# Kernel tuning notes

Hardware: AMD Instinct MI355X
Metric: run time of the kernel (lower is better)

The kernel has to match this reference:

```python
import jax, jax.numpy as jnp
import numpy as np

LN_EPS = 1e-5
NUM_EXPERTS = 8

def setup_inputs() -> dict:
    key = jax.random.key(0)
    ks = jax.random.split(key, 8)
    B, S, D = 8, 2048, 2048
    R = D // 4  # reduced_dim = 512
    E = NUM_EXPERTS
    scale1 = 1.0 / np.sqrt(D)
    scale2 = 1.0 / np.sqrt(R)
    return {
        "hidden_states": jax.random.normal(ks[0], (B, S, D), dtype=jnp.float32),
        "ln_gamma": jnp.ones((D,), dtype=jnp.float32),
        "ln_beta": jnp.zeros((D,), dtype=jnp.float32),
        "w1": jax.random.uniform(ks[1], (D, R), minval=-scale1, maxval=scale1, dtype=jnp.float32),
        "b1": jax.random.uniform(ks[2], (R,), minval=-scale1, maxval=scale1, dtype=jnp.float32),
        "w2": jax.random.uniform(ks[3], (R, R), minval=-scale2, maxval=scale2, dtype=jnp.float32),
        "b2": jax.random.uniform(ks[4], (R,), minval=-scale2, maxval=scale2, dtype=jnp.float32),
        "wr": jax.random.uniform(ks[5], (R, E), minval=-scale2, maxval=scale2, dtype=jnp.float32),
        "br": jax.random.uniform(ks[6], (E,), minval=-scale2, maxval=scale2, dtype=jnp.float32),
    }

def reference(hidden_states, ln_gamma, ln_beta, w1, b1, w2, b2, wr, br):
    # LayerNorm over last dim (eps matches torch default 1e-5)
    mu = jnp.mean(hidden_states, axis=-1, keepdims=True)
    var = jnp.mean(jnp.square(hidden_states - mu), axis=-1, keepdims=True)
    x = (hidden_states - mu) * jax.lax.rsqrt(var + LN_EPS) * ln_gamma + ln_beta
    # Linear -> GELU (exact, torch default) -> Linear
    h = jax.nn.gelu(jnp.einsum('bsd,dr->bsr', x, w1) + b1, approximate=False)
    t = jnp.einsum('bsr,rq->bsq', h, w2) + b2  # [B,S,R]
    batch_reduced = jnp.sum(t, axis=1)          # [B,R]
    router_logits = batch_reduced @ wr + br     # [B,E]
    # top-1 expert per batch element; one-hot targets via scatter
    expert_indices = jnp.argmax(router_logits, axis=-1)                 # [B]
    targets = jax.nn.one_hot(expert_indices, router_logits.shape[-1],
                             dtype=router_logits.dtype)                 # [B,E]
    # BCE-with-logits, mean over all elements: log(1+e^x) - x*t
    aux_loss = jnp.mean(jnp.logaddexp(0.0, router_logits) - router_logits * targets)
    # mode over batch of top-1 indices (torch .mode returns smallest on ties;
    # argmax of bincount picks the first/smallest max index -> matches)
    counts = jnp.sum(targets, axis=0)
    next_idx = jnp.argmax(counts)
    return aux_loss, next_idx
```

## Files before the change

kernel.cpp:

```cpp
#include <hip/hip_runtime.h>
#include <math.h>

#define D_DIM 2048
#define R_DIM 512
#define E_NUM 8
#define B_NUM 8
#define S_NUM 2048
#define M_DIM 16384
#define LN_EPS 1e-5f

typedef __attribute__((ext_vector_type(8))) short bf16x8;
typedef __attribute__((ext_vector_type(4))) float f32x4;

__device__ __forceinline__ unsigned short f2bf(float f) {
    unsigned u = __float_as_uint(f);
    return (unsigned short)((u + 0x7FFFu + ((u >> 16) & 1u)) >> 16);
}
__device__ __forceinline__ float bf2f(unsigned short h) {
    return __uint_as_float(((unsigned)h) << 16);
}

__device__ __forceinline__ void gload_lds16(const void* g, void* l) {
    __builtin_amdgcn_global_load_lds(
        (const __attribute__((address_space(1))) void*)g,
        (__attribute__((address_space(3))) void*)l, 16, 0, 0);
}

__global__ __launch_bounds__(256) void ln_split_kernel(float* __restrict__ x,
                                                       const float* __restrict__ gamma,
                                                       const float* __restrict__ beta) {
    __shared__ float sred[8];
    const int t = threadIdx.x;
    float* row = x + (size_t)blockIdx.x * D_DIM;
    const float4 v0  = ((const float4*)row)[t];
    const float4 v1  = ((const float4*)row)[t + 256];
    const float4 g0  = ((const float4*)gamma)[t];
    const float4 g1  = ((const float4*)gamma)[t + 256];
    const float4 be0 = ((const float4*)beta)[t];
    const float4 be1 = ((const float4*)beta)[t + 256];

    float s  = v0.x + v0.y + v0.z + v0.w + v1.x + v1.y + v1.z + v1.w;
    float sq = v0.x*v0.x + v0.y*v0.y + v0.z*v0.z + v0.w*v0.w
             + v1.x*v1.x + v1.y*v1.y + v1.z*v1.z + v1.w*v1.w;
#pragma unroll
    for (int off = 32; off > 0; off >>= 1) {
        s  += __shfl_down(s, off);
        sq += __shfl_down(sq, off);
    }
    if ((t & 63) == 0) { sred[(t >> 6) * 2] = s; sred[(t >> 6) * 2 + 1] = sq; }
    __syncthreads();
    s  = sred[0] + sred[2] + sred[4] + sred[6];
    sq = sred[1] + sred[3] + sred[5] + sred[7];
    const float mu  = s * (1.f / D_DIM);
    const float var = sq * (1.f / D_DIM) - mu * mu;
    const float rs  = rsqrtf(var + LN_EPS);

    ushort4 h0, h1;
    h0.x = f2bf(fmaf((v0.x - mu) * rs, g0.x, be0.x));
    h0.y = f2bf(fmaf((v0.y - mu) * rs, g0.y, be0.y));
    h0.z = f2bf(fmaf((v0.z - mu) * rs, g0.z, be0.z));
    h0.w = f2bf(fmaf((v0.w - mu) * rs, g0.w, be0.w));
    h1.x = f2bf(fmaf((v1.x - mu) * rs, g1.x, be1.x));
    h1.y = f2bf(fmaf((v1.y - mu) * rs, g1.y, be1.y));
    h1.z = f2bf(fmaf((v1.z - mu) * rs, g1.z, be1.z));
    h1.w = f2bf(fmaf((v1.w - mu) * rs, g1.w, be1.w));

    ushort4* rowu = (ushort4*)row;
    rowu[t]       = h0;
    rowu[t + 256] = h1;
}

__global__ __launch_bounds__(256) void wsplit_kernel(const float* __restrict__ w1,
                                                     unsigned short* __restrict__ wt_hi,
                                                     unsigned short* __restrict__ wt_lo) {
    const int tid = blockIdx.x * 256 + threadIdx.x;
    const int n  = tid >> 9;
    const int k4 = tid & 511;
    ushort4 h, l;
    unsigned short hh;
    float f;
    f = w1[(size_t)(k4 * 4 + 0) * R_DIM + n]; hh = f2bf(f); h.x = hh; l.x = f2bf(f - bf2f(hh));
    f = w1[(size_t)(k4 * 4 + 1) * R_DIM + n]; hh = f2bf(f); h.y = hh; l.y = f2bf(f - bf2f(hh));
    f = w1[(size_t)(k4 * 4 + 2) * R_DIM + n]; hh = f2bf(f); h.z = hh; l.z = f2bf(f - bf2f(hh));
    f = w1[(size_t)(k4 * 4 + 3) * R_DIM + n]; hh = f2bf(f); h.w = hh; l.w = f2bf(f - bf2f(hh));
    ((ushort4*)wt_hi)[(size_t)n * 512 + k4] = h;
    ((ushort4*)wt_lo)[(size_t)n * 512 + k4] = l;
}

#define BM 128
#define BN 128
#define BK 64

__global__ __launch_bounds__(256, 2) void gemm_kernel(
    const unsigned short* __restrict__ xs,
    const unsigned short* __restrict__ wt_hi,
    const unsigned short* __restrict__ wt_lo,
    const float* __restrict__ b1,
    float* __restrict__ hsum) {
    __shared__ __align__(16) unsigned short lds[3 * 8192];

    const int t = threadIdx.x, lane = t & 63, wid = t >> 6;
    const int xcd = blockIdx.x & 7, i0 = blockIdx.x >> 3;
    const int n0 = (xcd >> 1) * BN;
    const int m0 = ((xcd & 1) * 64 + i0) * BM;
    const int mw = wid >> 1, nw = wid & 1;
    const int fr = lane & 15, kg = lane >> 4, fr7 = lane & 7;

    f32x4 acc[4][4];
#pragma unroll
    for (int i = 0; i < 4; ++i)
#pragma unroll
        for (int j = 0; j < 4; ++j) acc[i][j] = (f32x4){0.f, 0.f, 0.f, 0.f};

    int srow[4], sgo[4], ldso[4];
#pragma unroll
    for (int ii = 0; ii < 4; ++ii) {
        const int idx = wid * 4 + ii;
        const int o = (idx << 10) + (lane << 4);
        const int r = o >> 7, sl = (o >> 4) & 7;
        srow[ii] = r;
        sgo[ii]  = ((sl ^ (r & 7)) << 4);
        ldso[ii] = (idx << 10);
    }

    int aoff[4], boff[4];
#pragma unroll
    for (int f = 0; f < 4; ++f) {
        aoff[f] = (mw * 64 + f * 16 + fr) * 128;
        boff[f] = (nw * 64 + f * 16 + fr) * 128;
    }
    const char* ldsb = (const char*)lds;

    for (int k0b = 0; k0b < D_DIM * 2; k0b += BK * 2) {
        __syncthreads();
#pragma unroll
        for (int ii = 0; ii < 4; ++ii) {
            const char* a  = (const char*)xs    + (size_t)(m0 + srow[ii]) * 8192 + k0b + sgo[ii];
            const char* bh = (const char*)wt_hi + (size_t)(n0 + srow[ii]) * 4096 + k0b + sgo[ii];
            const char* bl = (const char*)wt_lo + (size_t)(n0 + srow[ii]) * 4096 + k0b + sgo[ii];
            gload_lds16(a,  (char*)lds +     0 + ldso[ii]);
            gload_lds16(bh, (char*)lds + 16384 + ldso[ii]);
            gload_lds16(bl, (char*)lds + 32768 + ldso[ii]);
        }
        __syncthreads();
#pragma unroll
        for (int kk = 0; kk < 2; ++kk) {
            const int sw = ((kk * 4 + kg) ^ fr7) << 4;
            bf16x8 ah[4], bh[4], bl[4];
#pragma unroll
            for (int f = 0; f < 4; ++f) {
                ah[f] = *(const bf16x8*)(ldsb +     0 + aoff[f] + sw);
                bh[f] = *(const bf16x8*)(ldsb + 16384 + boff[f] + sw);
                bl[f] = *(const bf16x8*)(ldsb + 32768 + boff[f] + sw);
            }
#pragma unroll
            for (int i = 0; i < 4; ++i)
#pragma unroll
                for (int j = 0; j < 4; ++j) {
                    acc[i][j] = __builtin_amdgcn_mfma_f32_16x16x32_bf16(ah[i], bh[j], acc[i][j], 0, 0, 0);
                    acc[i][j] = __builtin_amdgcn_mfma_f32_16x16x32_bf16(ah[i], bl[j], acc[i][j], 0, 0, 0);
                }
        }
    }

    __syncthreads();
    float* red = (float*)lds;
    float pn[4];
#pragma unroll
    for (int j = 0; j < 4; ++j) pn[j] = 0.f;
#pragma unroll
    for (int j = 0; j < 4; ++j) {
        const float bb = b1[n0 + nw * 64 + j * 16 + fr];
#pragma unroll
        for (int i = 0; i < 4; ++i)
#pragma unroll
            for (int r = 0; r < 4; ++r) {
                const float y = acc[i][j][r] + bb;
                pn[j] += 0.5f * y * (1.f + erff(y * 0.70710678118654752f));
            }
    }
#pragma unroll
    for (int j = 0; j < 4; ++j)
        red[(wid * 4 + kg) * 64 + j * 16 + fr] = pn[j];
    __syncthreads();
    if (t < 128) {
        const int nw2 = t >> 6, cl = t & 63;
        float s2 = 0.f;
#pragma unroll
        for (int mw2 = 0; mw2 < 2; ++mw2)
#pragma unroll
            for (int g = 0; g < 4; ++g)
                s2 += red[((mw2 * 2 + nw2) * 4 + g) * 64 + cl];
        atomicAdd(&hsum[(m0 >> 11) * R_DIM + n0 + t], s2);
    }
}

__global__ void router1_kernel(const float* __restrict__ hsum,
                               const float* __restrict__ w2,
                               float* __restrict__ brd) {
    const int q  = blockIdx.x * 64 + threadIdx.x;
    const int r0 = blockIdx.y * 64;
    float acc[8] = {0, 0, 0, 0, 0, 0, 0, 0};
    for (int r = r0 + threadIdx.y; r < r0 + 64; r += 4) {
        const float w = w2[(size_t)r * R_DIM + q];
#pragma unroll
        for (int b = 0; b < 8; ++b) acc[b] = fmaf(hsum[b * R_DIM + r], w, acc[b]);
    }
    __shared__ float sred[4][8][64];
#pragma unroll
    for (int b = 0; b < 8; ++b) sred[threadIdx.y][b][threadIdx.x] = acc[b];
    __syncthreads();
    if (threadIdx.y == 0) {
#pragma unroll
        for (int b = 0; b < 8; ++b) {
            float s = sred[0][b][threadIdx.x] + sred[1][b][threadIdx.x]
                    + sred[2][b][threadIdx.x] + sred[3][b][threadIdx.x];
            atomicAdd(&brd[b * R_DIM + q], s);
        }
    }
}

__global__ void router2_kernel(const float* __restrict__ brd,
                               const float* __restrict__ b2,
                               const float* __restrict__ wr,
                               const float* __restrict__ br,
                               float* __restrict__ out) {
    __shared__ float lg[64];
    const int t = threadIdx.x;
    const int b = t >> 3, e = t & 7;
    float s = br[e];
    for (int q = 0; q < R_DIM; ++q) {
        const float v = fmaf((float)S_NUM, b2[q], brd[b * R_DIM + q]);
        s = fmaf(v, wr[q * E_NUM + e], s);
    }
    lg[t] = s;
    __syncthreads();
    if (t == 0) {
        int cnt[8] = {0, 0, 0, 0, 0, 0, 0, 0};
        float loss = 0.f;
        for (int bb = 0; bb < 8; ++bb) {
            int best = 0;
            float bv = lg[bb * 8];
            for (int ee = 1; ee < 8; ++ee)
                if (lg[bb * 8 + ee] > bv) { bv = lg[bb * 8 + ee]; best = ee; }
            cnt[best]++;
            for (int ee = 0; ee < 8; ++ee) {
                const float xv = lg[bb * 8 + ee];
                loss += fmaxf(xv, 0.f) + log1pf(expf(-fabsf(xv))) - (ee == best ? xv : 0.f);
            }
        }
        out[0] = loss * (1.f / 64.f);
        int ni = 0;
        for (int ee = 1; ee < 8; ++ee)
            if (cnt[ee] > cnt[ni]) ni = ee;
        out[1] = (float)ni;
    }
}

extern "C" void kernel_launch(void* const* d_in, const int* in_sizes, int n_in,
                              void* d_out, int out_size, void* d_ws, size_t ws_size,
                              hipStream_t stream) {
    float* x           = (float*)d_in[0];
    const float* gamma = (const float*)d_in[1];
    const float* beta  = (const float*)d_in[2];
    const float* w1    = (const float*)d_in[3];
    const float* b1    = (const float*)d_in[4];
    const float* w2    = (const float*)d_in[5];
    const float* b2    = (const float*)d_in[6];
    const float* wr    = (const float*)d_in[7];
    const float* br    = (const float*)d_in[8];
    float* out = (float*)d_out;
    float* ws  = (float*)d_ws;

    float* hsum = ws;
    float* brd  = ws + 4096;
    unsigned short* wt_hi = (unsigned short*)(ws + 8192);
    unsigned short* wt_lo = wt_hi + (size_t)R_DIM * D_DIM;

    hipMemsetAsync(ws, 0, 8192 * sizeof(float), stream);
    ln_split_kernel<<<dim3(M_DIM), dim3(256), 0, stream>>>(x, gamma, beta);
    wsplit_kernel<<<dim3(1024), dim3(256), 0, stream>>>(w1, wt_hi, wt_lo);
    gemm_kernel<<<dim3(512), dim3(256), 0, stream>>>(
        (const unsigned short*)x, wt_hi, wt_lo, b1, hsum);
    router1_kernel<<<dim3(8, 8), dim3(64, 4), 0, stream>>>(hsum, w2, brd);
    router2_kernel<<<dim3(1), dim3(64), 0, stream>>>(brd, b2, wr, br, out);
}
```

Baseline: 334.5 us.

## Drop bf16 hi/lo weight split, fuse prep kernels, parallelize router reduction

The weight matrix is now rounded to a single bf16 copy instead of a hi/lo pair, which halves the MFMA count, the B-tile loads and the LDS footprint in the GEMM. LayerNorm, the weight conversion and workspace zeroing are merged into one prep kernel, replacing a memset and two launches. The b2 bias is folded into router1, and router2 splits its dot products across 8 thread groups. The cost is lower weight precision, which could flip an argmax in routing when logits are close.

```diff
diff --git a/kernel.cpp b/kernel.cpp
--- a/kernel.cpp
+++ b/kernel.cpp
@@ -16,9 +16,6 @@
     unsigned u = __float_as_uint(f);
     return (unsigned short)((u + 0x7FFFu + ((u >> 16) & 1u)) >> 16);
 }
-__device__ __forceinline__ float bf2f(unsigned short h) {
-    return __uint_as_float(((unsigned)h) << 16);
-}
 
 __device__ __forceinline__ void gload_lds16(const void* g, void* l) {
     __builtin_amdgcn_global_load_lds(
@@ -26,65 +23,65 @@
         (__attribute__((address_space(3))) void*)l, 16, 0, 0);
 }
 
-__global__ __launch_bounds__(256) void ln_split_kernel(float* __restrict__ x,
-                                                       const float* __restrict__ gamma,
-                                                       const float* __restrict__ beta) {
-    __shared__ float sred[8];
+__global__ __launch_bounds__(256) void prep_kernel(float* __restrict__ x,
+                                                   const float* __restrict__ gamma,
+                                                   const float* __restrict__ beta,
+                                                   const float* __restrict__ w1,
+                                                   unsigned short* __restrict__ wt,
+                                                   float* __restrict__ zbuf) {
     const int t = threadIdx.x;
-    float* row = x + (size_t)blockIdx.x * D_DIM;
-    const float4 v0  = ((const float4*)row)[t];
-    const float4 v1  = ((const float4*)row)[t + 256];
-    const float4 g0  = ((const float4*)gamma)[t];
-    const float4 g1  = ((const float4*)gamma)[t + 256];
-    const float4 be0 = ((const float4*)beta)[t];
-    const float4 be1 = ((const float4*)beta)[t + 256];
-
-    float s  = v0.x + v0.y + v0.z + v0.w + v1.x + v1.y + v1.z + v1.w;
-    float sq = v0.x*v0.x + v0.y*v0.y + v0.z*v0.z + v0.w*v0.w
-             + v1.x*v1.x + v1.y*v1.y + v1.z*v1.z + v1.w*v1.w;
-#pragma unroll
-    for (int off = 32; off > 0; off >>= 1) {
-        s  += __shfl_down(s, off);
-        sq += __shfl_down(sq, off);
-    }
-    if ((t & 63) == 0) { sred[(t >> 6) * 2] = s; sred[(t >> 6) * 2 + 1] = sq; }
-    __syncthreads();
-    s  = sred[0] + sred[2] + sred[4] + sred[6];
-    sq = sred[1] + sred[3] + sred[5] + sred[7];
-    const float mu  = s * (1.f / D_DIM);
-    const float var = sq * (1.f / D_DIM) - mu * mu;
-    const float rs  = rsqrtf(var + LN_EPS);
-
-    ushort4 h0, h1;
-    h0.x = f2bf(fmaf((v0.x - mu) * rs, g0.x, be0.x));
-    h0.y = f2bf(fmaf((v0.y - mu) * rs, g0.y, be0.y));
-    h0.z = f2bf(fmaf((v0.z - mu) * rs, g0.z, be0.z));
-    h0.w = f2bf(fmaf((v0.w - mu) * rs, g0.w, be0.w));
-    h1.x = f2bf(fmaf((v1.x - mu) * rs, g1.x, be1.x));
-    h1.y = f2bf(fmaf((v1.y - mu) * rs, g1.y, be1.y));
-    h1.z = f2bf(fmaf((v1.z - mu) * rs, g1.z, be1.z));
-    h1.w = f2bf(fmaf((v1.w - mu) * rs, g1.w, be1.w));
-
-    ushort4* rowu = (ushort4*)row;
-    rowu[t]       = h0;
-    rowu[t + 256] = h1;
-}
-
-__global__ __launch_bounds__(256) void wsplit_kernel(const float* __restrict__ w1,
-                                                     unsigned short* __restrict__ wt_hi,
-                                                     unsigned short* __restrict__ wt_lo) {
-    const int tid = blockIdx.x * 256 + threadIdx.x;
-    const int n  = tid >> 9;
-    const int k4 = tid & 511;
-    ushort4 h, l;
-    unsigned short hh;
-    float f;
-    f = w1[(size_t)(k4 * 4 + 0) * R_DIM + n]; hh = f2bf(f); h.x = hh; l.x = f2bf(f - bf2f(hh));
-    f = w1[(size_t)(k4 * 4 + 1) * R_DIM + n]; hh = f2bf(f); h.y = hh; l.y = f2bf(f - bf2f(hh));
-    f = w1[(size_t)(k4 * 4 + 2) * R_DIM + n]; hh = f2bf(f); h.z = hh; l.z = f2bf(f - bf2f(hh));
-    f = w1[(size_t)(k4 * 4 + 3) * R_DIM + n]; hh = f2bf(f); h.w = hh; l.w = f2bf(f - bf2f(hh));
-    ((ushort4*)wt_hi)[(size_t)n * 512 + k4] = h;
-    ((ushort4*)wt_lo)[(size_t)n * 512 + k4] = l;
+    if (blockIdx.x < M_DIM) {
+        __shared__ float sred[8];
+        float* row = x + (size_t)blockIdx.x * D_DIM;
+        const float4 v0  = ((const float4*)row)[t];
+        const float4 v1  = ((const float4*)row)[t + 256];
+        const float4 g0  = ((const float4*)gamma)[t];
+        const float4 g1  = ((const float4*)gamma)[t + 256];
+        const float4 be0 = ((const float4*)beta)[t];
+        const float4 be1 = ((const float4*)beta)[t + 256];
+
+        float s  = v0.x + v0.y + v0.z + v0.w + v1.x + v1.y + v1.z + v1.w;
+        float sq = v0.x*v0.x + v0.y*v0.y + v0.z*v0.z + v0.w*v0.w
+                 + v1.x*v1.x + v1.y*v1.y + v1.z*v1.z + v1.w*v1.w;
+#pragma unroll
+        for (int off = 32; off > 0; off >>= 1) {
+            s  += __shfl_down(s, off);
+            sq += __shfl_down(sq, off);
+        }
+        if ((t & 63) == 0) { sred[(t >> 6) * 2] = s; sred[(t >> 6) * 2 + 1] = sq; }
+        __syncthreads();
+        s  = sred[0] + sred[2] + sred[4] + sred[6];
+        sq = sred[1] + sred[3] + sred[5] + sred[7];
+        const float mu  = s * (1.f / D_DIM);
+        const float var = sq * (1.f / D_DIM) - mu * mu;
+        const float rs  = rsqrtf(var + LN_EPS);
+
+        ushort4 h0, h1;
+        h0.x = f2bf(fmaf((v0.x - mu) * rs, g0.x, be0.x));
+        h0.y = f2bf(fmaf((v0.y - mu) * rs, g0.y, be0.y));
+        h0.z = f2bf(fmaf((v0.z - mu) * rs, g0.z, be0.z));
+        h0.w = f2bf(fmaf((v0.w - mu) * rs, g0.w, be0.w));
+        h1.x = f2bf(fmaf((v1.x - mu) * rs, g1.x, be1.x));
+        h1.y = f2bf(fmaf((v1.y - mu) * rs, g1.y, be1.y));
+        h1.z = f2bf(fmaf((v1.z - mu) * rs, g1.z, be1.z));
+        h1.w = f2bf(fmaf((v1.w - mu) * rs, g1.w, be1.w));
+
+        ushort4* rowu = (ushort4*)row;
+        rowu[t]       = h0;
+        rowu[t + 256] = h1;
+    } else if (blockIdx.x < M_DIM + 1024) {
+        const int tid = (blockIdx.x - M_DIM) * 256 + t;
+        const int n  = tid >> 9;
+        const int k4 = tid & 511;
+        ushort4 h;
+        h.x = f2bf(w1[(size_t)(k4 * 4 + 0) * R_DIM + n]);
+        h.y = f2bf(w1[(size_t)(k4 * 4 + 1) * R_DIM + n]);
+        h.z = f2bf(w1[(size_t)(k4 * 4 + 2) * R_DIM + n]);
+        h.w = f2bf(w1[(size_t)(k4 * 4 + 3) * R_DIM + n]);
+        ((ushort4*)wt)[(size_t)n * 512 + k4] = h;
+    } else {
+        zbuf[(blockIdx.x - M_DIM - 1024) * 256 + t] = 0.f;
+    }
 }
 
 #define BM 128
@@ -93,11 +90,10 @@
 
 __global__ __launch_bounds__(256, 2) void gemm_kernel(
     const unsigned short* __restrict__ xs,
-    const unsigned short* __restrict__ wt_hi,
-    const unsigned short* __restrict__ wt_lo,
+    const unsigned short* __restrict__ wt,
     const float* __restrict__ b1,
     float* __restrict__ hsum) {
-    __shared__ __align__(16) unsigned short lds[3 * 8192];
+    __shared__ __align__(16) unsigned short lds[2 * 8192];
 
     const int t = threadIdx.x, lane = t & 63, wid = t >> 6;
     const int xcd = blockIdx.x & 7, i0 = blockIdx.x >> 3;
@@ -135,31 +131,26 @@
         __syncthreads();
 #pragma unroll
         for (int ii = 0; ii < 4; ++ii) {
-            const char* a  = (const char*)xs    + (size_t)(m0 + srow[ii]) * 8192 + k0b + sgo[ii];
-            const char* bh = (const char*)wt_hi + (size_t)(n0 + srow[ii]) * 4096 + k0b + sgo[ii];
-            const char* bl = (const char*)wt_lo + (size_t)(n0 + srow[ii]) * 4096 + k0b + sgo[ii];
-            gload_lds16(a,  (char*)lds +     0 + ldso[ii]);
-            gload_lds16(bh, (char*)lds + 16384 + ldso[ii]);
-            gload_lds16(bl, (char*)lds + 32768 + ldso[ii]);
+            const char* a = (const char*)xs + (size_t)(m0 + srow[ii]) * 8192 + k0b + sgo[ii];
+            const char* b = (const char*)wt + (size_t)(n0 + srow[ii]) * 4096 + k0b + sgo[ii];
+            gload_lds16(a, (char*)lds +     0 + ldso[ii]);
+            gload_lds16(b, (char*)lds + 16384 + ldso[ii]);
         }
         __syncthreads();
 #pragma unroll
         for (int kk = 0; kk < 2; ++kk) {
             const int sw = ((kk * 4 + kg) ^ fr7) << 4;
-            bf16x8 ah[4], bh[4], bl[4];
+            bf16x8 ah[4], bh[4];
 #pragma unroll
             for (int f = 0; f < 4; ++f) {
                 ah[f] = *(const bf16x8*)(ldsb +     0 + aoff[f] + sw);
                 bh[f] = *(const bf16x8*)(ldsb + 16384 + boff[f] + sw);
-                bl[f] = *(const bf16x8*)(ldsb + 32768 + boff[f] + sw);
             }
 #pragma unroll
             for (int i = 0; i < 4; ++i)
 #pragma unroll
-                for (int j = 0; j < 4; ++j) {
+                for (int j = 0; j < 4; ++j)
                     acc[i][j] = __builtin_amdgcn_mfma_f32_16x16x32_bf16(ah[i], bh[j], acc[i][j], 0, 0, 0);
-                    acc[i][j] = __builtin_amdgcn_mfma_f32_16x16x32_bf16(ah[i], bl[j], acc[i][j], 0, 0, 0);
-                }
         }
     }
 
@@ -197,6 +188,7 @@
 
 __global__ void router1_kernel(const float* __restrict__ hsum,
                                const float* __restrict__ w2,
+                               const float* __restrict__ b2,
                                float* __restrict__ brd) {
     const int q  = blockIdx.x * 64 + threadIdx.x;
     const int r0 = blockIdx.y * 64;
@@ -211,31 +203,38 @@
     for (int b = 0; b < 8; ++b) sred[threadIdx.y][b][threadIdx.x] = acc[b];
     __syncthreads();
     if (threadIdx.y == 0) {
+        const float bias2 = (blockIdx.y == 0) ? (float)S_NUM * b2[q] : 0.f;
 #pragma unroll
         for (int b = 0; b < 8; ++b) {
             float s = sred[0][b][threadIdx.x] + sred[1][b][threadIdx.x]
-                    + sred[2][b][threadIdx.x] + sred[3][b][threadIdx.x];
+                    + sred[2][b][threadIdx.x] + sred[3][b][threadIdx.x] + bias2;
             atomicAdd(&brd[b * R_DIM + q], s);
         }
     }
 }
 
 __global__ void router2_kernel(const float* __restrict__ brd,
-                               const float* __restrict__ b2,
                                const float* __restrict__ wr,
                                const float* __restrict__ br,
                                float* __restrict__ out) {
+    __shared__ float part[8][64];
     __shared__ float lg[64];
-    const int t = threadIdx.x;
-    const int b = t >> 3, e = t & 7;
-    float s = br[e];
-    for (int q = 0; q < R_DIM; ++q) {
-        const float v = fmaf((float)S_NUM, b2[q], brd[b * R_DIM + q]);
-        s = fmaf(v, wr[q * E_NUM + e], s);
-    }
-    lg[t] = s;
-    __syncthreads();
-    if (t == 0) {
+    const int te = threadIdx.x;
+    const int qg = threadIdx.y;
+    const int b = te >> 3, e = te & 7;
+    float s = 0.f;
+    for (int q = qg; q < R_DIM; q += 8)
+        s = fmaf(brd[b * R_DIM + q], wr[q * E_NUM + e], s);
+    part[qg][te] = s;
+    __syncthreads();
+    if (qg == 0) {
+        float v = br[e];
+#pragma unroll
+        for (int g = 0; g < 8; ++g) v += part[g][te];
+        lg[te] = v;
+    }
+    __syncthreads();
+    if (te == 0 && qg == 0) {
         int cnt[8] = {0, 0, 0, 0, 0, 0, 0, 0};
         float loss = 0.f;
         for (int bb = 0; bb < 8; ++bb) {
@@ -274,14 +273,12 @@
 
     float* hsum = ws;
     float* brd  = ws + 4096;
-    unsigned short* wt_hi = (unsigned short*)(ws + 8192);
-    unsigned short* wt_lo = wt_hi + (size_t)R_DIM * D_DIM;
-
-    hipMemsetAsync(ws, 0, 8192 * sizeof(float), stream);
-    ln_split_kernel<<<dim3(M_DIM), dim3(256), 0, stream>>>(x, gamma, beta);
-    wsplit_kernel<<<dim3(1024), dim3(256), 0, stream>>>(w1, wt_hi, wt_lo);
+    unsigned short* wt = (unsigned short*)(ws + 8192);
+
+    prep_kernel<<<dim3(M_DIM + 1024 + 32), dim3(256), 0, stream>>>(
+        x, gamma, beta, w1, wt, ws);
     gemm_kernel<<<dim3(512), dim3(256), 0, stream>>>(
-        (const unsigned short*)x, wt_hi, wt_lo, b1, hsum);
-    router1_kernel<<<dim3(8, 8), dim3(64, 4), 0, stream>>>(hsum, w2, brd);
-    router2_kernel<<<dim3(1), dim3(64), 0, stream>>>(brd, b2, wr, br, out);
-}
+        (const unsigned short*)x, wt, b1, hsum);
+    router1_kernel<<<dim3(8, 8), dim3(64, 4), 0, stream>>>(hsum, w2, b2, brd);
+    router2_kernel<<<dim3(1), dim3(64, 8), 0, stream>>>(brd, wr, br, out);
+}
```

Result: faster. 307.9 us (-8.0%).
